# Kernel optimization log

Hardware: AMD Instinct MI355X
Metric: run time of the kernel (lower is better)

The kernel has to match this reference:

```python
import jax, jax.numpy as jnp
import numpy as np

B, IN, H = 16384, 1024, 1024


def setup_inputs() -> dict:
    key = jax.random.key(0)
    ks = jax.random.split(key, 7)
    s_in = 1.0 / np.sqrt(IN)
    s_h = 1.0 / np.sqrt(H)
    return {
        "x": jax.random.normal(ks[0], (B, IN), jnp.float32),
        "h0": jax.random.normal(ks[1], (B, H), jnp.float32),
        "c0": jax.random.normal(ks[2], (B, H), jnp.float32),
        # gate order along leading dim: f, i, o, g
        "wi": jax.random.uniform(ks[3], (4, H, IN), jnp.float32, -s_in, s_in),
        "bi": jax.random.uniform(ks[4], (4, H), jnp.float32, -s_in, s_in),
        "wh": jax.random.uniform(ks[5], (4, H, H), jnp.float32, -s_h, s_h),
        "bh": jax.random.uniform(ks[6], (4, H), jnp.float32, -s_h, s_h),
    }


def reference(x, h0, c0, wi, bi, wh, bh):
    # pre-activations for all 4 gates in two fused GEMMs: [b, 4, h]
    z = (jnp.einsum("bi,ghi->bgh", x, wi) + bi
         + jnp.einsum("bj,ghj->bgh", h0, wh) + bh)
    f = jax.nn.sigmoid(z[:, 0])   # forget gate
    i = jax.nn.sigmoid(z[:, 1])   # input gate
    o = jax.nn.sigmoid(z[:, 2])   # output gate
    g = jnp.tanh(z[:, 3])         # candidates
    ct = f * c0 + i * g
    ht = o * jnp.tanh(ct)
    return ht, ct
```

## Files before the change

kernel.cpp:

```cpp
#include <hip/hip_runtime.h>
#include <hip/hip_bf16.h>
#include <stdint.h>

#define B_ROWS 16384
#define K_DIM  2048
#define H_DIM  1024
#define N_DIM  4096
#define KB     (K_DIM * 2)
#define NT     (K_DIM / 64)
#define BUFSZ  65536u

using f32x4  = __attribute__((ext_vector_type(4))) float;
using bf16x8 = __attribute__((ext_vector_type(8))) __bf16;

__device__ __forceinline__ unsigned short f2bf(float f) {
    union { float f; unsigned u; } v; v.f = f;
    unsigned r = v.u + 0x7fffu + ((v.u >> 16) & 1u);
    return (unsigned short)(r >> 16);
}

__device__ __forceinline__ void gload16(const void* g, const void* l) {
    __builtin_amdgcn_global_load_lds(
        (const __attribute__((address_space(1))) void*)g,
        (__attribute__((address_space(3))) void*)l,
        16, 0, 0);
}

__device__ __forceinline__ float rcp1p(float e) {
    return __builtin_amdgcn_rcpf(1.f + e);
}

__global__ void pack_a_kernel(const float* __restrict__ x, const float* __restrict__ h0,
                              unsigned short* __restrict__ A) {
    int tid = blockIdx.x * 256 + threadIdx.x;
    int64_t idx = (int64_t)tid * 4;
    int b = (int)(idx >> 11);
    int k = (int)(idx & 2047);
    const float* src = (k < 1024) ? (x + (int64_t)b * 1024 + k)
                                  : (h0 + (int64_t)b * 1024 + (k - 1024));
    float4 v = *(const float4*)src;
    ushort4 o;
    o.x = f2bf(v.x); o.y = f2bf(v.y); o.z = f2bf(v.z); o.w = f2bf(v.w);
    *(ushort4*)(A + idx) = o;
}

__global__ void pack_w_kernel(const float* __restrict__ wi, const float* __restrict__ wh,
                              const float* __restrict__ bi, const float* __restrict__ bh,
                              unsigned short* __restrict__ W, float* __restrict__ bias) {
    int tid = blockIdx.x * 256 + threadIdx.x;
    int64_t idx = (int64_t)tid * 4;
    int r = (int)(idx >> 11);
    int k = (int)(idx & 2047);
    int h = r >> 2, g = r & 3;
    const float* src = (k < 1024)
        ? (wi + (int64_t)g * 1048576 + (int64_t)h * 1024 + k)
        : (wh + (int64_t)g * 1048576 + (int64_t)h * 1024 + (k - 1024));
    float4 v = *(const float4*)src;
    ushort4 o;
    o.x = f2bf(v.x); o.y = f2bf(v.y); o.z = f2bf(v.z); o.w = f2bf(v.w);
    *(ushort4*)(W + idx) = o;
    if (k == 0) bias[r] = bi[g * 1024 + h] + bh[g * 1024 + h];
}


#define SCHED0  __builtin_amdgcn_sched_barrier(0)
#define FENCE   asm volatile("" ::: "memory")
#define BAR     __builtin_amdgcn_s_barrier()

#define PH_PRE  do { FENCE; BAR; \
                     asm volatile("s_waitcnt lgkmcnt(0)" ::: "memory"); \
                     SCHED0; __builtin_amdgcn_s_setprio(1); } while (0)
#define PH_POST do { __builtin_amdgcn_s_setprio(0); SCHED0; FENCE; BAR; } while (0)
#define PH_POST_V do { __builtin_amdgcn_s_setprio(0); SCHED0; \
                       asm volatile("s_waitcnt vmcnt(4)" ::: "memory"); \
                       SCHED0; FENCE; BAR; } while (0)

__global__ __launch_bounds__(512, 2) void lstm_gemm_fused(
    const unsigned short* __restrict__ A, const unsigned short* __restrict__ W,
    const float* __restrict__ bias, const float* __restrict__ c0,
    float* __restrict__ ht, float* __restrict__ ct)
{
    __shared__ char sm[131072];

    const int tid = threadIdx.x;
    const int l   = tid & 63;
    const int w   = tid >> 6;
    const int wm  = w >> 2;
    const int wn  = w & 3;

    const int bid = blockIdx.x;
    const int nid = (bid & 7) * 128 + (bid >> 3);
    const int bm  = nid >> 4;
    const int bn  = nid & 15;

    f32x4 acc[8][4];
#pragma unroll
    for (int i = 0; i < 8; ++i)
#pragma unroll
        for (int j = 0; j < 4; ++j) acc[i][j] = (f32x4){0.f, 0.f, 0.f, 0.f};

    const int srow = w * 16 + (l >> 2);
    const int scb  = ((l & 3) << 4) ^ (l & 32);
    const char* Asrc = (const char*)A + (size_t)(bm * 256 + srow) * KB + scb;
    const char* Wsrc = (const char*)W + (size_t)(bn * 256 + srow) * KB + scb;
    const uint32_t wL = (uint32_t)w * 1024u;

#define STAGE_A(KK, BOFF) do { \
    gload16(Asrc + (KK) * 64,            sm + (BOFF) + (KK) * 16384u + wL); \
    gload16(Asrc + (KK) * 64 + 128 * KB, sm + (BOFF) + (KK) * 16384u + 8192u + wL); \
} while (0)
#define STAGE_B(KK, BOFF) do { \
    gload16(Wsrc + (KK) * 64,            sm + (BOFF) + 32768u + (KK) * 16384u + wL); \
    gload16(Wsrc + (KK) * 64 + 128 * KB, sm + (BOFF) + 32768u + (KK) * 16384u + 8192u + wL); \
} while (0)

    const int rr = l & 15, kg = l >> 4;
    const uint32_t loff = (uint32_t)rr * 64u + (((uint32_t)kg * 16u) ^ (uint32_t)((rr & 8) << 2));
    const uint32_t Ard = (uint32_t)wm * 8192u + loff;
    const uint32_t Brd = 32768u + (uint32_t)wn * 4096u + loff;

    bf16x8 aL[4], aH[4], bb0[4], bb1[4];

#define RD_A4(BOFF, KK, MB, ARR) do { \
    _Pragma("unroll") \
    for (int i_ = 0; i_ < 4; ++i_) \
        ARR[i_] = *(const bf16x8*)(sm + (BOFF) + (KK) * 16384u + Ard + ((MB) + i_) * 1024u); \
} while (0)
#define RD_B4(BOFF, KK, BRR) do { \
    _Pragma("unroll") \
    for (int i_ = 0; i_ < 4; ++i_) \
        BRR[i_] = *(const bf16x8*)(sm + (BOFF) + (KK) * 16384u + Brd + i_ * 1024u); \
} while (0)

#define MFMA16H(ARR, MB, BRR) do { \
    _Pragma("unroll") \
    for (int mf_ = 0; mf_ < 4; ++mf_) \
        _Pragma("unroll") \
        for (int nf_ = 0; nf_ < 4; ++nf_) \
            acc[(MB) + mf_][nf_] = __builtin_amdgcn_mfma_f32_16x16x32_bf16( \
                ARR[mf_], BRR[nf_], acc[(MB) + mf_][nf_], 0, 0, 0); \
} while (0)

    STAGE_A(0, 0u); STAGE_B(0, 0u);
    STAGE_A(1, 0u); STAGE_B(1, 0u);
    Asrc += 128; Wsrc += 128;
    asm volatile("s_waitcnt vmcnt(4)" ::: "memory");
    SCHED0; FENCE; BAR;

#define DO_TILE(CUR, NXT) do { \
     \
    RD_A4(CUR, 0, 0, aL); RD_B4(CUR, 0, bb0); \
    STAGE_A(0, NXT); \
    PH_PRE; MFMA16H(aL, 0, bb0); PH_POST; \
     \
    RD_A4(CUR, 0, 4, aH); \
    STAGE_B(0, NXT); \
    PH_PRE; MFMA16H(aH, 4, bb0); PH_POST_V; \
     \
    RD_A4(CUR, 1, 0, aL); RD_B4(CUR, 1, bb1); \
    STAGE_A(1, NXT); \
    PH_PRE; MFMA16H(aL, 0, bb1); PH_POST; \
     \
    RD_A4(CUR, 1, 4, aH); \
    STAGE_B(1, NXT); \
    PH_PRE; MFMA16H(aH, 4, bb1); PH_POST_V; \
    Asrc += 128; Wsrc += 128; \
} while (0)

#pragma unroll 1
    for (int tt = 0; tt < NT; tt += 2) {
        DO_TILE(0u, BUFSZ);
        DO_TILE(BUFSZ, 0u);
    }

    asm volatile("s_waitcnt vmcnt(0) lgkmcnt(0)" ::: "memory");
    FENCE; BAR;

    float* ep = (float*)(void*)sm + w * 1088;
    const int hbase = bn * 64 + wn * 16;
    const int rbase = bm * 256 + wm * 128;

#pragma unroll
    for (int mf = 0; mf < 8; ++mf) {
#pragma unroll
        for (int nf = 0; nf < 4; ++nf)
#pragma unroll
            for (int r = 0; r < 4; ++r)
                ep[((l >> 4) * 4 + r) * 68 + nf * 16 + (l & 15)] = acc[mf][nf][r];

#pragma unroll
        for (int it = 0; it < 4; ++it) {
            const int row = (l >> 4) + it * 4;
            const int hs  = l & 15;
            f32x4 z = *(const f32x4*)(ep + row * 68 + hs * 4);
            const int hg = hbase + hs;
            const float4 bz = ((const float4*)bias)[hg];
            const int brow = rbase + mf * 16 + row;

            float zf = z.x + bz.x;
            float zi = z.y + bz.y;
            float zo = z.z + bz.z;
            float zg = z.w + bz.w;

            float fg = rcp1p(__expf(-zf));
            float ig = rcp1p(__expf(-zi));
            float og = rcp1p(__expf(-zo));
            float gg = 2.f * rcp1p(__expf(-2.f * zg)) - 1.f;

            int64_t oi = (int64_t)brow * H_DIM + hg;
            float c  = fg * c0[oi] + ig * gg;
            float hh = og * (2.f * rcp1p(__expf(-2.f * c)) - 1.f);
            ct[oi] = c;
            ht[oi] = hh;
        }
    }
}

extern "C" void kernel_launch(void* const* d_in, const int* in_sizes, int n_in,
                              void* d_out, int out_size, void* d_ws, size_t ws_size,
                              hipStream_t stream) {
    const float* x  = (const float*)d_in[0];
    const float* h0 = (const float*)d_in[1];
    const float* c0 = (const float*)d_in[2];
    const float* wi = (const float*)d_in[3];
    const float* bi = (const float*)d_in[4];
    const float* wh = (const float*)d_in[5];
    const float* bh = (const float*)d_in[6];

    float* ht = (float*)d_out;
    float* ct = ht + (int64_t)B_ROWS * H_DIM;

    char* ws = (char*)d_ws;
    unsigned short* A  = (unsigned short*)ws;
    unsigned short* Wp = (unsigned short*)(ws + (64u << 20));
    float*          bs = (float*)(ws + (80u << 20));

    pack_a_kernel<<<32768, 256, 0, stream>>>(x, h0, A);
    pack_w_kernel<<<8192, 256, 0, stream>>>(wi, wh, bi, bh, Wp, bs);

    lstm_gemm_fused<<<1024, 512, 0, stream>>>(A, Wp, bs, c0, ht, ct);
}
```

Baseline: 313.9 us.

## Switch GEMM to 32x32x16 MFMA tiles and merge pipeline phases

Replaces the 16x16x32 bf16 MFMA inner loop with 32x32x16 MFMAs, reorganizing the LDS fragment reads and accumulators into 4x2 f32x16 tiles. Each K sub-tile now runs as one phase instead of two, which halves the number of barriers per tile. The epilogue is rewritten for the 32x32 accumulator layout. The larger MFMA needs fewer LDS reads per flop and fewer instructions, but the bigger phases may overlap global loads less well, and the new LDS access pattern may change bank conflicts.

After: 344.0 us. 1.1x slower.

```diff
diff --git a/kernel.cpp b/kernel.cpp
--- a/kernel.cpp
+++ b/kernel.cpp
@@ -10,8 +10,9 @@
 #define NT     (K_DIM / 64)
 #define BUFSZ  65536u
 
-using f32x4  = __attribute__((ext_vector_type(4))) float;
-using bf16x8 = __attribute__((ext_vector_type(8))) __bf16;
+using f32x4   = __attribute__((ext_vector_type(4))) float;
+using f32x16  = __attribute__((ext_vector_type(16))) float;
+using bf16x8  = __attribute__((ext_vector_type(8))) __bf16;
 
 __device__ __forceinline__ unsigned short f2bf(float f) {
     union { float f; unsigned u; } v; v.f = f;
@@ -70,7 +71,6 @@
 #define PH_PRE  do { FENCE; BAR; \
                      asm volatile("s_waitcnt lgkmcnt(0)" ::: "memory"); \
                      SCHED0; __builtin_amdgcn_s_setprio(1); } while (0)
-#define PH_POST do { __builtin_amdgcn_s_setprio(0); SCHED0; FENCE; BAR; } while (0)
 #define PH_POST_V do { __builtin_amdgcn_s_setprio(0); SCHED0; \
                        asm volatile("s_waitcnt vmcnt(4)" ::: "memory"); \
                        SCHED0; FENCE; BAR; } while (0)
@@ -93,11 +93,13 @@
     const int bm  = nid >> 4;
     const int bn  = nid & 15;
 
-    f32x4 acc[8][4];
-#pragma unroll
-    for (int i = 0; i < 8; ++i)
-#pragma unroll
-        for (int j = 0; j < 4; ++j) acc[i][j] = (f32x4){0.f, 0.f, 0.f, 0.f};
+    f32x16 acc[4][2];
+#pragma unroll
+    for (int i = 0; i < 4; ++i)
+#pragma unroll
+        for (int j = 0; j < 2; ++j)
+#pragma unroll
+            for (int e = 0; e < 16; ++e) acc[i][j][e] = 0.f;
 
     const int srow = w * 16 + (l >> 2);
     const int scb  = ((l & 3) << 4) ^ (l & 32);
@@ -114,31 +116,39 @@
     gload16(Wsrc + (KK) * 64 + 128 * KB, sm + (BOFF) + 32768u + (KK) * 16384u + 8192u + wL); \
 } while (0)
 
-    const int rr = l & 15, kg = l >> 4;
-    const uint32_t loff = (uint32_t)rr * 64u + (((uint32_t)kg * 16u) ^ (uint32_t)((rr & 8) << 2));
-    const uint32_t Ard = (uint32_t)wm * 8192u + loff;
-    const uint32_t Brd = 32768u + (uint32_t)wn * 4096u + loff;
-
-    bf16x8 aL[4], aH[4], bb0[4], bb1[4];
-
-#define RD_A4(BOFF, KK, MB, ARR) do { \
+    const uint32_t sub   = ((uint32_t)(l >> 4) & 1u) * 1024u;
+    const uint32_t lofA  = (uint32_t)(l & 15) * 64u + ((uint32_t)(l >> 5)) * 16u;
+    const uint32_t xr    = (uint32_t)((l & 8) << 2);
+    const uint32_t lane0 = sub + lofA + xr;
+    const uint32_t lane1 = sub + lofA + (xr ^ 32u);
+    const uint32_t ArdB  = (uint32_t)wm * 8192u;
+    const uint32_t BrdB  = 32768u + (uint32_t)wn * 4096u;
+
+    bf16x8 af[4][2], bf[2][2];
+
+#define RD_PHASE(BOFF, KK) do { \
+    const uint32_t cb_ = (BOFF) + (KK) * 16384u; \
     _Pragma("unroll") \
-    for (int i_ = 0; i_ < 4; ++i_) \
-        ARR[i_] = *(const bf16x8*)(sm + (BOFF) + (KK) * 16384u + Ard + ((MB) + i_) * 1024u); \
-} while (0)
-#define RD_B4(BOFF, KK, BRR) do { \
+    for (int mf_ = 0; mf_ < 4; ++mf_) { \
+        af[mf_][0] = *(const bf16x8*)(sm + cb_ + ArdB + mf_ * 2048u + lane0); \
+        af[mf_][1] = *(const bf16x8*)(sm + cb_ + ArdB + mf_ * 2048u + lane1); \
+    } \
     _Pragma("unroll") \
-    for (int i_ = 0; i_ < 4; ++i_) \
-        BRR[i_] = *(const bf16x8*)(sm + (BOFF) + (KK) * 16384u + Brd + i_ * 1024u); \
-} while (0)
-
-#define MFMA16H(ARR, MB, BRR) do { \
+    for (int nf_ = 0; nf_ < 2; ++nf_) { \
+        bf[nf_][0] = *(const bf16x8*)(sm + cb_ + BrdB + nf_ * 2048u + lane0); \
+        bf[nf_][1] = *(const bf16x8*)(sm + cb_ + BrdB + nf_ * 2048u + lane1); \
+    } \
+} while (0)
+
+#define MFMA16 do { \
     _Pragma("unroll") \
-    for (int mf_ = 0; mf_ < 4; ++mf_) \
+    for (int ks_ = 0; ks_ < 2; ++ks_) \
         _Pragma("unroll") \
-        for (int nf_ = 0; nf_ < 4; ++nf_) \
-            acc[(MB) + mf_][nf_] = __builtin_amdgcn_mfma_f32_16x16x32_bf16( \
-                ARR[mf_], BRR[nf_], acc[(MB) + mf_][nf_], 0, 0, 0); \
+        for (int mf_ = 0; mf_ < 4; ++mf_) \
+            _Pragma("unroll") \
+            for (int nf_ = 0; nf_ < 2; ++nf_) \
+                acc[mf_][nf_] = __builtin_amdgcn_mfma_f32_32x32x16_bf16( \
+                    af[mf_][ks_], bf[nf_][ks_], acc[mf_][nf_], 0, 0, 0); \
 } while (0)
 
     STAGE_A(0, 0u); STAGE_B(0, 0u);
@@ -149,21 +159,13 @@
 
 #define DO_TILE(CUR, NXT) do { \
      \
-    RD_A4(CUR, 0, 0, aL); RD_B4(CUR, 0, bb0); \
-    STAGE_A(0, NXT); \
-    PH_PRE; MFMA16H(aL, 0, bb0); PH_POST; \
+    RD_PHASE(CUR, 0); \
+    STAGE_A(0, NXT); STAGE_B(0, NXT); \
+    PH_PRE; MFMA16; PH_POST_V; \
      \
-    RD_A4(CUR, 0, 4, aH); \
-    STAGE_B(0, NXT); \
-    PH_PRE; MFMA16H(aH, 4, bb0); PH_POST_V; \
-     \
-    RD_A4(CUR, 1, 0, aL); RD_B4(CUR, 1, bb1); \
-    STAGE_A(1, NXT); \
-    PH_PRE; MFMA16H(aL, 0, bb1); PH_POST; \
-     \
-    RD_A4(CUR, 1, 4, aH); \
-    STAGE_B(1, NXT); \
-    PH_PRE; MFMA16H(aH, 4, bb1); PH_POST_V; \
+    RD_PHASE(CUR, 1); \
+    STAGE_A(1, NXT); STAGE_B(1, NXT); \
+    PH_PRE; MFMA16; PH_POST_V; \
     Asrc += 128; Wsrc += 128; \
 } while (0)
 
@@ -176,26 +178,31 @@
     asm volatile("s_waitcnt vmcnt(0) lgkmcnt(0)" ::: "memory");
     FENCE; BAR;
 
-    float* ep = (float*)(void*)sm + w * 1088;
+    float* ep = (float*)(void*)sm + w * 2176;
     const int hbase = bn * 64 + wn * 16;
     const int rbase = bm * 256 + wm * 128;
-
-#pragma unroll
-    for (int mf = 0; mf < 8; ++mf) {
-#pragma unroll
-        for (int nf = 0; nf < 4; ++nf)
-#pragma unroll
-            for (int r = 0; r < 4; ++r)
-                ep[((l >> 4) * 4 + r) * 68 + nf * 16 + (l & 15)] = acc[mf][nf][r];
-
-#pragma unroll
-        for (int it = 0; it < 4; ++it) {
-            const int row = (l >> 4) + it * 4;
-            const int hs  = l & 15;
-            f32x4 z = *(const f32x4*)(ep + row * 68 + hs * 4);
-            const int hg = hbase + hs;
+    const int rl = (l >> 5) * 4;
+    const int cl = l & 31;
+
+#pragma unroll
+    for (int mf = 0; mf < 4; ++mf) {
+#pragma unroll
+        for (int nf = 0; nf < 2; ++nf)
+#pragma unroll
+            for (int g = 0; g < 4; ++g)
+#pragma unroll
+                for (int ri = 0; ri < 4; ++ri)
+                    ep[(ri + g * 8 + rl) * 68 + nf * 32 + cl] = acc[mf][nf][g * 4 + ri];
+
+#pragma unroll
+        for (int it = 0; it < 8; ++it) {
+            const int c   = it * 64 + l;
+            const int row = c >> 4;
+            const int hq  = c & 15;
+            f32x4 z = *(const f32x4*)(ep + row * 68 + hq * 4);
+            const int hg = hbase + hq;
             const float4 bz = ((const float4*)bias)[hg];
-            const int brow = rbase + mf * 16 + row;
+            const int brow = rbase + mf * 32 + row;
 
             float zf = z.x + bz.x;
             float zi = z.y + bz.y;
@@ -208,9 +215,9 @@
             float gg = 2.f * rcp1p(__expf(-2.f * zg)) - 1.f;
 
             int64_t oi = (int64_t)brow * H_DIM + hg;
-            float c  = fg * c0[oi] + ig * gg;
-            float hh = og * (2.f * rcp1p(__expf(-2.f * c)) - 1.f);
-            ct[oi] = c;
+            float cc = fg * c0[oi] + ig * gg;
+            float hh = og * (2.f * rcp1p(__expf(-2.f * cc)) - 1.f);
+            ct[oi] = cc;
             ht[oi] = hh;
         }
     }
```

## Prefetch LDS fragments one phase ahead and halve barriers in GEMM loop

Applied to the files above, without the earlier changes.

Restructures the software pipeline of the fused LSTM GEMM. LDS fragment reads for the next MFMA phase are now issued before the current phase's MFMAs, using extra register buffers and partial lgkmcnt waits. This lets shared-memory reads overlap matrix math. It also drops the sched_barriers and the second barrier per phase, keeping one barrier per phase with vmcnt waits placed before it. The trade-off is higher register pressure from six fragment arrays, and correctness now depends on careful ordering of global-to-LDS writes against the prefetched reads.

Result: faster. 306.5 us (-2.4%).

```diff
diff --git a/kernel.cpp b/kernel.cpp
--- a/kernel.cpp
+++ b/kernel.cpp
@@ -8,7 +8,8 @@
 #define N_DIM  4096
 #define KB     (K_DIM * 2)
 #define NT     (K_DIM / 64)
-#define BUFSZ  65536u
+#define BUF0   0u
+#define BUF1   65536u
 
 using f32x4  = __attribute__((ext_vector_type(4))) float;
 using bf16x8 = __attribute__((ext_vector_type(8))) __bf16;
@@ -63,17 +64,13 @@
 }
 
 
-#define SCHED0  __builtin_amdgcn_sched_barrier(0)
 #define FENCE   asm volatile("" ::: "memory")
-#define BAR     __builtin_amdgcn_s_barrier()
-
-#define PH_PRE  do { FENCE; BAR; \
-                     asm volatile("s_waitcnt lgkmcnt(0)" ::: "memory"); \
-                     SCHED0; __builtin_amdgcn_s_setprio(1); } while (0)
-#define PH_POST do { __builtin_amdgcn_s_setprio(0); SCHED0; FENCE; BAR; } while (0)
-#define PH_POST_V do { __builtin_amdgcn_s_setprio(0); SCHED0; \
-                       asm volatile("s_waitcnt vmcnt(4)" ::: "memory"); \
-                       SCHED0; FENCE; BAR; } while (0)
+#define BARRIER do { FENCE; __builtin_amdgcn_s_barrier(); FENCE; } while (0)
+#define VM2     asm volatile("s_waitcnt vmcnt(2)" ::: "memory")
+#define LGKM4   asm volatile("s_waitcnt lgkmcnt(4)" ::: "memory")
+#define LGKM8   asm volatile("s_waitcnt lgkmcnt(8)" ::: "memory")
+#define SP1     __builtin_amdgcn_s_setprio(1)
+#define SP0     __builtin_amdgcn_s_setprio(0)
 
 __global__ __launch_bounds__(512, 2) void lstm_gemm_fused(
     const unsigned short* __restrict__ A, const unsigned short* __restrict__ W,
@@ -113,13 +110,14 @@
     gload16(Wsrc + (KK) * 64,            sm + (BOFF) + 32768u + (KK) * 16384u + wL); \
     gload16(Wsrc + (KK) * 64 + 128 * KB, sm + (BOFF) + 32768u + (KK) * 16384u + 8192u + wL); \
 } while (0)
+#define BUMP do { Asrc += 128; Wsrc += 128; } while (0)
 
     const int rr = l & 15, kg = l >> 4;
     const uint32_t loff = (uint32_t)rr * 64u + (((uint32_t)kg * 16u) ^ (uint32_t)((rr & 8) << 2));
     const uint32_t Ard = (uint32_t)wm * 8192u + loff;
     const uint32_t Brd = 32768u + (uint32_t)wn * 4096u + loff;
 
-    bf16x8 aL[4], aH[4], bb0[4], bb1[4];
+    bf16x8 aL0[4], aH0[4], aL1[4], aH1[4], bb0[4], bb1[4];
 
 #define RD_A4(BOFF, KK, MB, ARR) do { \
     _Pragma("unroll") \
@@ -141,40 +139,41 @@
                 ARR[mf_], BRR[nf_], acc[(MB) + mf_][nf_], 0, 0, 0); \
 } while (0)
 
-    STAGE_A(0, 0u); STAGE_B(0, 0u);
-    STAGE_A(1, 0u); STAGE_B(1, 0u);
-    Asrc += 128; Wsrc += 128;
+    STAGE_A(0, BUF0); STAGE_B(0, BUF0);
+    STAGE_A(1, BUF0); STAGE_B(1, BUF0);
+    BUMP;
     asm volatile("s_waitcnt vmcnt(4)" ::: "memory");
-    SCHED0; FENCE; BAR;
+    BARRIER;
+    RD_A4(BUF0, 0, 0, aL0); RD_B4(BUF0, 0, bb0);
 
 #define DO_TILE(CUR, NXT) do { \
      \
-    RD_A4(CUR, 0, 0, aL); RD_B4(CUR, 0, bb0); \
+    RD_A4(CUR, 0, 4, aH0); \
     STAGE_A(0, NXT); \
-    PH_PRE; MFMA16H(aL, 0, bb0); PH_POST; \
-     \
-    RD_A4(CUR, 0, 4, aH); \
+    VM2; BARRIER; LGKM4; SP1; MFMA16H(aL0, 0, bb0); SP0; \
+     \
+    RD_A4(CUR, 1, 0, aL1); RD_B4(CUR, 1, bb1); \
     STAGE_B(0, NXT); \
-    PH_PRE; MFMA16H(aH, 4, bb0); PH_POST_V; \
-     \
-    RD_A4(CUR, 1, 0, aL); RD_B4(CUR, 1, bb1); \
+    BARRIER; LGKM8; SP1; MFMA16H(aH0, 4, bb0); SP0; \
+     \
+    RD_A4(CUR, 1, 4, aH1); \
     STAGE_A(1, NXT); \
-    PH_PRE; MFMA16H(aL, 0, bb1); PH_POST; \
-     \
-    RD_A4(CUR, 1, 4, aH); \
+    VM2; BARRIER; LGKM4; SP1; MFMA16H(aL1, 0, bb1); SP0; \
+     \
+    RD_A4(NXT, 0, 0, aL0); RD_B4(NXT, 0, bb0); \
     STAGE_B(1, NXT); \
-    PH_PRE; MFMA16H(aH, 4, bb1); PH_POST_V; \
-    Asrc += 128; Wsrc += 128; \
+    BUMP; \
+    BARRIER; LGKM8; SP1; MFMA16H(aH1, 4, bb1); SP0; \
 } while (0)
 
 #pragma unroll 1
     for (int tt = 0; tt < NT; tt += 2) {
-        DO_TILE(0u, BUFSZ);
-        DO_TILE(BUFSZ, 0u);
+        DO_TILE(BUF0, BUF1);
+        DO_TILE(BUF1, BUF0);
     }
 
     asm volatile("s_waitcnt vmcnt(0) lgkmcnt(0)" ::: "memory");
-    FENCE; BAR;
+    BARRIER;
 
     float* ep = (float*)(void*)sm + w * 1088;
     const int hbase = bn * 64 + wn * 16;
```

## Shrink GEMM block tile from 256x256 to 128x128 with four waves

Applied to the files above, without the earlier changes.

Reduces the fused LSTM GEMM block tile from 256x256 (8 waves, 128 KB LDS) to 128x128 (4 waves, 64 KB LDS), quadrupling the grid to 4096 blocks. Each wave now computes a 64x64 sub-tile with one merged A/B read-and-stage phase per k-slice instead of two half phases. The aim is more blocks for better load balance and occupancy, at the cost of lower arithmetic intensity per block and more global/L2 traffic for A and W.

New measurement: 412.4 us. +31.4%, slower.

```diff
diff --git a/kernel.cpp b/kernel.cpp
--- a/kernel.cpp
+++ b/kernel.cpp
@@ -8,7 +8,8 @@
 #define N_DIM  4096
 #define KB     (K_DIM * 2)
 #define NT     (K_DIM / 64)
-#define BUFSZ  65536u
+#define BUF0   0u
+#define BUF1   32768u
 
 using f32x4  = __attribute__((ext_vector_type(4))) float;
 using bf16x8 = __attribute__((ext_vector_type(8))) __bf16;
@@ -63,125 +64,115 @@
 }
 
 
-#define SCHED0  __builtin_amdgcn_sched_barrier(0)
 #define FENCE   asm volatile("" ::: "memory")
 #define BAR     __builtin_amdgcn_s_barrier()
+#define SCHED0  __builtin_amdgcn_sched_barrier(0)
 
 #define PH_PRE  do { FENCE; BAR; \
                      asm volatile("s_waitcnt lgkmcnt(0)" ::: "memory"); \
                      SCHED0; __builtin_amdgcn_s_setprio(1); } while (0)
-#define PH_POST do { __builtin_amdgcn_s_setprio(0); SCHED0; FENCE; BAR; } while (0)
 #define PH_POST_V do { __builtin_amdgcn_s_setprio(0); SCHED0; \
                        asm volatile("s_waitcnt vmcnt(4)" ::: "memory"); \
                        SCHED0; FENCE; BAR; } while (0)
 
-__global__ __launch_bounds__(512, 2) void lstm_gemm_fused(
+__global__ __launch_bounds__(256, 2) void lstm_gemm_fused(
     const unsigned short* __restrict__ A, const unsigned short* __restrict__ W,
     const float* __restrict__ bias, const float* __restrict__ c0,
     float* __restrict__ ht, float* __restrict__ ct)
 {
-    __shared__ char sm[131072];
+    __shared__ char sm[65536];
 
     const int tid = threadIdx.x;
     const int l   = tid & 63;
     const int w   = tid >> 6;
-    const int wm  = w >> 2;
-    const int wn  = w & 3;
+    const int wm  = w >> 1;
+    const int wn  = w & 1;
 
     const int bid = blockIdx.x;
-    const int nid = (bid & 7) * 128 + (bid >> 3);
-    const int bm  = nid >> 4;
-    const int bn  = nid & 15;
-
-    f32x4 acc[8][4];
-#pragma unroll
-    for (int i = 0; i < 8; ++i)
+    const int nid = (bid & 7) * 512 + (bid >> 3);
+    const int bm  = nid >> 5;
+    const int bn  = nid & 31;
+
+    f32x4 acc[4][4];
+#pragma unroll
+    for (int i = 0; i < 4; ++i)
 #pragma unroll
         for (int j = 0; j < 4; ++j) acc[i][j] = (f32x4){0.f, 0.f, 0.f, 0.f};
 
     const int srow = w * 16 + (l >> 2);
     const int scb  = ((l & 3) << 4) ^ (l & 32);
-    const char* Asrc = (const char*)A + (size_t)(bm * 256 + srow) * KB + scb;
-    const char* Wsrc = (const char*)W + (size_t)(bn * 256 + srow) * KB + scb;
+    const char* Asrc = (const char*)A + (size_t)(bm * 128 + srow) * KB + scb;
+    const char* Wsrc = (const char*)W + (size_t)(bn * 128 + srow) * KB + scb;
     const uint32_t wL = (uint32_t)w * 1024u;
 
 #define STAGE_A(KK, BOFF) do { \
-    gload16(Asrc + (KK) * 64,            sm + (BOFF) + (KK) * 16384u + wL); \
-    gload16(Asrc + (KK) * 64 + 128 * KB, sm + (BOFF) + (KK) * 16384u + 8192u + wL); \
+    gload16(Asrc + (KK) * 64,           sm + (BOFF) + (KK) * 8192u + wL); \
+    gload16(Asrc + (KK) * 64 + 64 * KB, sm + (BOFF) + (KK) * 8192u + 4096u + wL); \
 } while (0)
 #define STAGE_B(KK, BOFF) do { \
-    gload16(Wsrc + (KK) * 64,            sm + (BOFF) + 32768u + (KK) * 16384u + wL); \
-    gload16(Wsrc + (KK) * 64 + 128 * KB, sm + (BOFF) + 32768u + (KK) * 16384u + 8192u + wL); \
-} while (0)
+    gload16(Wsrc + (KK) * 64,           sm + (BOFF) + 16384u + (KK) * 8192u + wL); \
+    gload16(Wsrc + (KK) * 64 + 64 * KB, sm + (BOFF) + 16384u + (KK) * 8192u + 4096u + wL); \
+} while (0)
+#define BUMP do { Asrc += 128; Wsrc += 128; } while (0)
 
     const int rr = l & 15, kg = l >> 4;
     const uint32_t loff = (uint32_t)rr * 64u + (((uint32_t)kg * 16u) ^ (uint32_t)((rr & 8) << 2));
-    const uint32_t Ard = (uint32_t)wm * 8192u + loff;
-    const uint32_t Brd = 32768u + (uint32_t)wn * 4096u + loff;
-
-    bf16x8 aL[4], aH[4], bb0[4], bb1[4];
-
-#define RD_A4(BOFF, KK, MB, ARR) do { \
+    const uint32_t Ard = (uint32_t)wm * 4096u + loff;
+    const uint32_t Brd = 16384u + (uint32_t)wn * 4096u + loff;
+
+    bf16x8 af[4], bf[4];
+
+#define RD_PHASE(BOFF, KK) do { \
     _Pragma("unroll") \
     for (int i_ = 0; i_ < 4; ++i_) \
-        ARR[i_] = *(const bf16x8*)(sm + (BOFF) + (KK) * 16384u + Ard + ((MB) + i_) * 1024u); \
-} while (0)
-#define RD_B4(BOFF, KK, BRR) do { \
+        af[i_] = *(const bf16x8*)(sm + (BOFF) + (KK) * 8192u + Ard + i_ * 1024u); \
     _Pragma("unroll") \
     for (int i_ = 0; i_ < 4; ++i_) \
-        BRR[i_] = *(const bf16x8*)(sm + (BOFF) + (KK) * 16384u + Brd + i_ * 1024u); \
-} while (0)
-
-#define MFMA16H(ARR, MB, BRR) do { \
+        bf[i_] = *(const bf16x8*)(sm + (BOFF) + (KK) * 8192u + Brd + i_ * 1024u); \
+} while (0)
+
+#define MFMA16 do { \
     _Pragma("unroll") \
     for (int mf_ = 0; mf_ < 4; ++mf_) \
         _Pragma("unroll") \
         for (int nf_ = 0; nf_ < 4; ++nf_) \
-            acc[(MB) + mf_][nf_] = __builtin_amdgcn_mfma_f32_16x16x32_bf16( \
-                ARR[mf_], BRR[nf_], acc[(MB) + mf_][nf_], 0, 0, 0); \
-} while (0)
-
-    STAGE_A(0, 0u); STAGE_B(0, 0u);
-    STAGE_A(1, 0u); STAGE_B(1, 0u);
-    Asrc += 128; Wsrc += 128;
+            acc[mf_][nf_] = __builtin_amdgcn_mfma_f32_16x16x32_bf16( \
+                af[mf_], bf[nf_], acc[mf_][nf_], 0, 0, 0); \
+} while (0)
+
+    STAGE_A(0, BUF0); STAGE_B(0, BUF0);
+    STAGE_A(1, BUF0); STAGE_B(1, BUF0);
+    BUMP;
     asm volatile("s_waitcnt vmcnt(4)" ::: "memory");
     SCHED0; FENCE; BAR;
 
 #define DO_TILE(CUR, NXT) do { \
      \
-    RD_A4(CUR, 0, 0, aL); RD_B4(CUR, 0, bb0); \
-    STAGE_A(0, NXT); \
-    PH_PRE; MFMA16H(aL, 0, bb0); PH_POST; \
+    RD_PHASE(CUR, 0); \
+    STAGE_A(0, NXT); STAGE_B(0, NXT); \
+    PH_PRE; MFMA16; PH_POST_V; \
      \
-    RD_A4(CUR, 0, 4, aH); \
-    STAGE_B(0, NXT); \
-    PH_PRE; MFMA16H(aH, 4, bb0); PH_POST_V; \
-     \
-    RD_A4(CUR, 1, 0, aL); RD_B4(CUR, 1, bb1); \
-    STAGE_A(1, NXT); \
-    PH_PRE; MFMA16H(aL, 0, bb1); PH_POST; \
-     \
-    RD_A4(CUR, 1, 4, aH); \
-    STAGE_B(1, NXT); \
-    PH_PRE; MFMA16H(aH, 4, bb1); PH_POST_V; \
-    Asrc += 128; Wsrc += 128; \
+    RD_PHASE(CUR, 1); \
+    STAGE_A(1, NXT); STAGE_B(1, NXT); \
+    PH_PRE; MFMA16; PH_POST_V; \
+    BUMP; \
 } while (0)
 
 #pragma unroll 1
     for (int tt = 0; tt < NT; tt += 2) {
-        DO_TILE(0u, BUFSZ);
-        DO_TILE(BUFSZ, 0u);
+        DO_TILE(BUF0, BUF1);
+        DO_TILE(BUF1, BUF0);
     }
 
     asm volatile("s_waitcnt vmcnt(0) lgkmcnt(0)" ::: "memory");
     FENCE; BAR;
 
     float* ep = (float*)(void*)sm + w * 1088;
-    const int hbase = bn * 64 + wn * 16;
-    const int rbase = bm * 256 + wm * 128;
-
-#pragma unroll
-    for (int mf = 0; mf < 8; ++mf) {
+    const int hbase = bn * 32 + wn * 16;
+    const int rbase = bm * 128 + wm * 64;
+
+#pragma unroll
+    for (int mf = 0; mf < 4; ++mf) {
 #pragma unroll
         for (int nf = 0; nf < 4; ++nf)
 #pragma unroll
@@ -238,5 +229,5 @@
     pack_a_kernel<<<32768, 256, 0, stream>>>(x, h0, A);
     pack_w_kernel<<<8192, 256, 0, stream>>>(wi, wh, bi, bh, Wp, bs);
 
-    lstm_gemm_fused<<<1024, 512, 0, stream>>>(A, Wp, bs, c0, ht, ct);
-}
+    lstm_gemm_fused<<<4096, 256, 0, stream>>>(A, Wp, bs, c0, ht, ct);
+}
```
